# Kernel tuning notes

Hardware: AMD Instinct MI355X
Metric: run time of the kernel (lower is better)

## Reference

```python
import jax, jax.numpy as jnp
import numpy as np

N = 500_000          # total nodes (25000 graphs x 20 joints)
E = 800_000          # total edges (25000 graphs x 32 edges)
NUM_EDGES = 32       # edges per graph (module init arg)
IN_C = 128
OUT_C = 256
LN_EPS = 1e-5


def setup_inputs() -> dict:
    key = jax.random.key(0)
    ks = jax.random.split(key, 8)
    x = jax.random.normal(ks[0], (N, IN_C), dtype=jnp.float32)
    edge_index = jax.random.randint(ks[1], (2, E), 0, N, dtype=jnp.int64)
    # learned per-graph edge weights (init ones in torch; randomized positive here)
    edge_weights = jax.random.uniform(ks[2], (NUM_EDGES,), jnp.float32, 0.5, 1.5)
    W_gcn = jax.random.normal(ks[3], (IN_C, OUT_C), jnp.float32) / np.float32(np.sqrt(IN_C))
    b_gcn = jnp.zeros((OUT_C,), jnp.float32)
    W_res = jax.random.normal(ks[4], (IN_C, OUT_C), jnp.float32) / np.float32(np.sqrt(IN_C))
    b_res = jnp.zeros((OUT_C,), jnp.float32)
    gamma = jnp.ones((OUT_C,), jnp.float32)
    beta = jnp.zeros((OUT_C,), jnp.float32)
    return dict(x=x, edge_weights=edge_weights, W_gcn=W_gcn, b_gcn=b_gcn,
                W_res=W_res, b_res=b_res, gamma=gamma, beta=beta,
                edge_index=edge_index)


def reference(x, edge_weights, W_gcn, b_gcn, W_res, b_res, gamma, beta, edge_index):
    n = x.shape[0]
    e_tot = edge_index.shape[1]
    batch_size = e_tot // NUM_EDGES
    ew = jnp.tile(edge_weights, batch_size)            # repeated per-batch weights [E]
    row, col = edge_index[0], edge_index[1]            # source -> target

    # GCN symmetric normalization with implicit self loops (weight 1)
    deg = jax.ops.segment_sum(ew, col, num_segments=n) + 1.0   # [N]
    dinv = jax.lax.rsqrt(deg)                                   # [N]
    norm = dinv[row] * ew * dinv[col]                           # [E]

    xw = x @ W_gcn                                              # [N, OUT_C]
    agg = jax.ops.segment_sum(norm[:, None] * xw[row], col, num_segments=n)
    # self-loop contribution: norm_ii = dinv_i * 1 * dinv_i = 1/deg_i
    gcn_out = agg + xw * (dinv * dinv)[:, None] + b_gcn         # [N, OUT_C]

    res = x @ W_res + b_res                                     # residual Linear
    h = gcn_out + res

    mu = jnp.mean(h, axis=-1, keepdims=True)
    var = jnp.mean((h - mu) ** 2, axis=-1, keepdims=True)
    hn = (h - mu) * jax.lax.rsqrt(var + LN_EPS)
    return jax.nn.relu(hn * gamma + beta)
```

## Files before the change

kernel.cpp:

```cpp
#include <hip/hip_runtime.h>
#include <hip/hip_bf16.h>

typedef __attribute__((ext_vector_type(8))) short short8;
typedef __attribute__((ext_vector_type(8))) unsigned short ushort8;
typedef __attribute__((ext_vector_type(4))) float f32x4;
typedef unsigned short u16;
typedef unsigned long long u64;

#define IN_C 128
#define OUT_C 256
#define LN_EPS 1e-5f
#define CHUNK 512
#define WSCALE 1048576.0f

__device__ __forceinline__ u16 f2bf(float f) {
    __hip_bfloat16 h = __float2bfloat16(f);
    return __builtin_bit_cast(u16, h);
}

__global__ void k_zero(float4* __restrict__ p, int n4) {
    int i = blockIdx.x * 256 + threadIdx.x;
    if (i < n4) p[i] = make_float4(0.f, 0.f, 0.f, 0.f);
}

__global__ void k_count(const int* __restrict__ ei, const float* __restrict__ ew,
                        u64* __restrict__ pk, int E, int nbc,
                        const float* __restrict__ Wg, const float* __restrict__ Wr,
                        const float* __restrict__ bg, const float* __restrict__ br,
                        u16* __restrict__ wfrag, float* __restrict__ bc) {
    int b = blockIdx.x;
    if (b < nbc) {
        int e = b * 256 + threadIdx.x;
        if (e < E) {
            int c = ei[E + e];
            unsigned w = (unsigned)(ew[e & 31] * WSCALE + 0.5f);
            atomicAdd(&pk[c], (1ULL << 32) | (u64)w);
        }
        return;
    }
    int tid = (b - nbc) * 256 + threadIdx.x;
    if (tid < OUT_C) bc[tid] = bg[tid] + br[tid];
    if (tid >= 8192) return;
    int l = tid & 63;
    int t = (tid >> 6) & 15;
    int s = tid >> 10;
    int n = t * 16 + (l & 15);
    int k0 = s * 32 + (l >> 4) * 8;
    short8 pkk;
#pragma unroll
    for (int j = 0; j < 8; ++j) {
        int k = k0 + j;
        float w = (k < IN_C) ? Wg[k * OUT_C + n] : Wr[(k - IN_C) * OUT_C + n];
        pkk[j] = (short)f2bf(w);
    }
    reinterpret_cast<short8*>(wfrag)[tid] = pkk;
}

__global__ void k_scan1(const u64* __restrict__ pk, int* __restrict__ partial,
                        float* __restrict__ dinv, int n) {
    __shared__ int sm[256];
    int b = blockIdx.x, t = threadIdx.x;
    int base = b * 1024 + t * 4;
    int s = 0;
#pragma unroll
    for (int k = 0; k < 4; ++k) {
        int i = base + k;
        if (i < n) {
            u64 v = pk[i];
            s += (int)(v >> 32);
            dinv[i] = rsqrtf(1.0f + (float)(unsigned)(v & 0xffffffffULL) * (1.0f / WSCALE));
        }
    }
    sm[t] = s; __syncthreads();
    for (int m = 128; m > 0; m >>= 1) { if (t < m) sm[t] += sm[t + m]; __syncthreads(); }
    if (t == 0) partial[b] = sm[0];
}

__global__ void k_scan2(int* __restrict__ partial, int nb) {
    __shared__ int sm[512];
    int t = threadIdx.x;
    sm[t] = (t < nb) ? partial[t] : 0;
    __syncthreads();
    for (int d = 1; d < 512; d <<= 1) {
        int v = (t >= d) ? sm[t - d] : 0;
        __syncthreads();
        sm[t] += v;
        __syncthreads();
    }
    if (t < nb) partial[t] = (t == 0) ? 0 : sm[t - 1];
}

__global__ void k_scan3(const u64* __restrict__ pk, const int* __restrict__ partial,
                        int* __restrict__ off, int* __restrict__ cur, int n, int E) {
    __shared__ int sm[256];
    int b = blockIdx.x, t = threadIdx.x;
    int base = b * 1024 + t * 4;
    int c[4]; int s = 0;
#pragma unroll
    for (int k = 0; k < 4; ++k) {
        int i = base + k;
        c[k] = (i < n) ? (int)(pk[i] >> 32) : 0;
        s += c[k];
    }
    sm[t] = s; __syncthreads();
    for (int d = 1; d < 256; d <<= 1) {
        int v = (t >= d) ? sm[t - d] : 0;
        __syncthreads();
        sm[t] += v;
        __syncthreads();
    }
    int run = partial[b] + (sm[t] - s);
#pragma unroll
    for (int k = 0; k < 4; ++k) {
        int i = base + k;
        if (i < n) { off[i] = run; cur[i] = run; }
        run += c[k];
    }
    if (b == 0 && t == 0) off[n] = E;
}

__global__ void k_place(const int* __restrict__ ei, const float* __restrict__ ew,
                        const float* __restrict__ dinv, int* __restrict__ cur,
                        int2* __restrict__ rec2, int E) {
    int e = blockIdx.x * 256 + threadIdx.x;
    if (e >= E) return;
    int r = ei[e], c = ei[E + e];
    float nrm = dinv[r] * ew[e & 31] * dinv[c];
    int p = atomicAdd(&cur[c], 1);
    rec2[p] = make_int2(r, __float_as_int(nrm));
}

__global__ __launch_bounds__(512, 4) void k_gemm(
    const float4* __restrict__ x4, const float* __restrict__ dinv,
    const int* __restrict__ off, const int2* __restrict__ rec2g,
    const u16* __restrict__ wfrag, const float* __restrict__ bc,
    const float* __restrict__ gamma, const float* __restrict__ beta,
    float* __restrict__ out, int N) {

    __shared__ u16 A[32 * 264];
    __shared__ float red[8 * 32 * 2];
    __shared__ float fin[32 * 2];
    __shared__ int2 recs[CHUNK];

    const int tid = threadIdx.x;
    const int lane = tid & 63;
    const int wv = tid >> 6;
    const long r0 = (long)blockIdx.x * 32;

    const int trow = tid >> 4;
    const int tq = tid & 15;
    const long gr = r0 + trow;

    float ua[8];
    int p0 = 0, p1 = 0;
    {
        u16* xp = &A[trow * 264 + 128 + tq * 8];
        if (gr < N) {
            float d = dinv[gr];
            float d2 = d * d;
            const float4* xs = x4 + gr * 32 + tq * 2;
            float4 v0 = xs[0], v1 = xs[1];
            ushort4 x0, x1;
            x0.x = f2bf(v0.x); x0.y = f2bf(v0.y); x0.z = f2bf(v0.z); x0.w = f2bf(v0.w);
            x1.x = f2bf(v1.x); x1.y = f2bf(v1.y); x1.z = f2bf(v1.z); x1.w = f2bf(v1.w);
            *reinterpret_cast<ushort4*>(xp) = x0;
            *reinterpret_cast<ushort4*>(xp + 4) = x1;
            ua[0] = v0.x * d2; ua[1] = v0.y * d2; ua[2] = v0.z * d2; ua[3] = v0.w * d2;
            ua[4] = v1.x * d2; ua[5] = v1.y * d2; ua[6] = v1.z * d2; ua[7] = v1.w * d2;
            p0 = off[gr]; p1 = off[gr + 1];
        } else {
#pragma unroll
            for (int k = 0; k < 8; ++k) ua[k] = 0.f;
            ushort4 zz = {0, 0, 0, 0};
            *reinterpret_cast<ushort4*>(xp) = zz;
            *reinterpret_cast<ushort4*>(xp + 4) = zz;
        }
    }

    const int rend = (int)((r0 + 32 < N) ? (r0 + 32) : N);
    const int e0 = off[r0];
    const int e1 = off[rend];
    for (int cb = e0; cb < e1; cb += CHUNK) {
        const int ce = (cb + CHUNK < e1) ? (cb + CHUNK) : e1;
        __syncthreads();
        for (int i = tid; i < ce - cb; i += 512) recs[i] = rec2g[cb + i];
        __syncthreads();
        const int q0 = (p0 > cb) ? p0 : cb;
        const int q1 = (p1 < ce) ? p1 : ce;
        for (int p = q0; p < q1; p += 4) {
            const int nb = q1 - p;
            int sr[4]; float nr[4];
            float4 ga[4][2];
#pragma unroll
            for (int b = 0; b < 4; ++b) {
                if (b < nb) {
                    int2 rc = recs[p - cb + b];
                    sr[b] = rc.x;
                    nr[b] = __int_as_float(rc.y);
                }
            }
#pragma unroll
            for (int b = 0; b < 4; ++b) {
                if (b < nb) {
                    const float4* xr = x4 + (long)sr[b] * 32 + tq * 2;
                    ga[b][0] = xr[0];
                    ga[b][1] = xr[1];
                }
            }
#pragma unroll
            for (int b = 0; b < 4; ++b) {
                if (b < nb) {
                    ua[0] += nr[b] * ga[b][0].x; ua[1] += nr[b] * ga[b][0].y;
                    ua[2] += nr[b] * ga[b][0].z; ua[3] += nr[b] * ga[b][0].w;
                    ua[4] += nr[b] * ga[b][1].x; ua[5] += nr[b] * ga[b][1].y;
                    ua[6] += nr[b] * ga[b][1].z; ua[7] += nr[b] * ga[b][1].w;
                }
            }
        }
    }

    {
        ushort4 u0, u1;
        u0.x = f2bf(ua[0]); u0.y = f2bf(ua[1]); u0.z = f2bf(ua[2]); u0.w = f2bf(ua[3]);
        u1.x = f2bf(ua[4]); u1.y = f2bf(ua[5]); u1.z = f2bf(ua[6]); u1.w = f2bf(ua[7]);
        u16* up = &A[trow * 264 + tq * 8];
        *reinterpret_cast<ushort4*>(up) = u0;
        *reinterpret_cast<ushort4*>(up + 4) = u1;
    }
    __syncthreads();

    const short8* wf = reinterpret_cast<const short8*>(wfrag);
    short8 bfr[8][2];
#pragma unroll
    for (int s = 0; s < 8; ++s) {
#pragma unroll
        for (int t = 0; t < 2; ++t)
            bfr[s][t] = wf[(s * 16 + (wv * 2 + t)) * 64 + lane];
    }

    f32x4 acc[2][2];
#pragma unroll
    for (int m = 0; m < 2; ++m)
#pragma unroll
        for (int t = 0; t < 2; ++t) acc[m][t] = (f32x4){0.f, 0.f, 0.f, 0.f};

    const int arowb = lane & 15;
    const int koff = (lane >> 4) * 8;
#pragma unroll
    for (int s = 0; s < 8; ++s) {
#pragma unroll
        for (int m = 0; m < 2; ++m) {
            short8 af = *reinterpret_cast<const short8*>(
                &A[(m * 16 + arowb) * 264 + s * 32 + koff]);
#pragma unroll
            for (int t = 0; t < 2; ++t)
                acc[m][t] = __builtin_amdgcn_mfma_f32_16x16x32_bf16(af, bfr[s][t], acc[m][t], 0, 0, 0);
        }
    }

    const int ncol = lane & 15;
    const int g = lane >> 4;
    const float bc0 = bc[wv * 32 + ncol];
    const float bc1 = bc[wv * 32 + 16 + ncol];
#pragma unroll
    for (int m = 0; m < 2; ++m) {
#pragma unroll
        for (int j = 0; j < 4; ++j) {
            float v0 = acc[m][0][j] + bc0;
            float v1 = acc[m][1][j] + bc1;
            acc[m][0][j] = v0;
            acc[m][1][j] = v1;
            float s = v0 + v1;
            float q = v0 * v0 + v1 * v1;
#pragma unroll
            for (int msk = 1; msk < 16; msk <<= 1) {
                s += __shfl_xor(s, msk);
                q += __shfl_xor(q, msk);
            }
            if (ncol == 0) {
                int row = m * 16 + g * 4 + j;
                red[(wv * 32 + row) * 2 + 0] = s;
                red[(wv * 32 + row) * 2 + 1] = q;
            }
        }
    }
    __syncthreads();
    if (tid < 64) {
        int row = tid >> 1, q = tid & 1;
        float t = 0.f;
#pragma unroll
        for (int w = 0; w < 8; ++w) t += red[(w * 32 + row) * 2 + q];
        fin[row * 2 + q] = t;
    }
    __syncthreads();

    const float gv0 = gamma[wv * 32 + ncol], bv0 = beta[wv * 32 + ncol];
    const float gv1 = gamma[wv * 32 + 16 + ncol], bv1 = beta[wv * 32 + 16 + ncol];
#pragma unroll
    for (int m = 0; m < 2; ++m) {
#pragma unroll
        for (int j = 0; j < 4; ++j) {
            int row = m * 16 + g * 4 + j;
            long rr = r0 + row;
            if (rr < N) {
                float mean = fin[row * 2] * (1.f / 256.f);
                float var = fin[row * 2 + 1] * (1.f / 256.f) - mean * mean;
                float rstd = rsqrtf(var + LN_EPS);
                float o0 = (acc[m][0][j] - mean) * rstd * gv0 + bv0;
                float o1 = (acc[m][1][j] - mean) * rstd * gv1 + bv1;
                float* op = out + rr * (long)OUT_C + wv * 32 + ncol;
                op[0]  = fmaxf(o0, 0.f);
                op[16] = fmaxf(o1, 0.f);
            }
        }
    }
}

extern "C" void kernel_launch(void* const* d_in, const int* in_sizes, int n_in,
                              void* d_out, int out_size, void* d_ws, size_t ws_size,
                              hipStream_t stream) {
    const float* x    = (const float*)d_in[0];
    const float* ew   = (const float*)d_in[1];
    const float* Wg   = (const float*)d_in[2];
    const float* bg   = (const float*)d_in[3];
    const float* Wr   = (const float*)d_in[4];
    const float* br   = (const float*)d_in[5];
    const float* gm   = (const float*)d_in[6];
    const float* bt   = (const float*)d_in[7];
    const int*   ei   = (const int*)d_in[8];

    const int N = in_sizes[0] / IN_C;
    const int E = in_sizes[8] / 2;
    const int NB1 = (N + 1023) / 1024;
    const int NBC = (E + 255) / 256;

    int2*  rec2 = (int2*)d_ws;
    u64*   pk   = (u64*)(rec2 + E);
    float* dinv = (float*)(pk + N);
    int*   off  = (int*)(dinv + N);
    int*   cur  = off + N + 1;
    int*   part = cur + N;
    u16*   wfrag = (u16*)(part + 512);
    float* bc   = (float*)(wfrag + 65536);

    const int n4 = (2 * N + 3) / 4;
    k_zero<<<(n4 + 255) / 256, 256, 0, stream>>>((float4*)pk, n4);
    k_count<<<NBC + 32, 256, 0, stream>>>(ei, ew, pk, E, NBC,
                                          Wg, Wr, bg, br, wfrag, bc);
    k_scan1<<<NB1, 256, 0, stream>>>(pk, part, dinv, N);
    k_scan2<<<1, 512, 0, stream>>>(part, NB1);
    k_scan3<<<NB1, 256, 0, stream>>>(pk, part, off, cur, N, E);
    k_place<<<(E + 255) / 256, 256, 0, stream>>>(ei, ew, dinv, cur, rec2, E);
    k_gemm<<<(N + 31) / 32, 512, 0, stream>>>((const float4*)x, dinv, off, rec2,
                                              wfrag, bc, gm, bt, (float*)d_out, N);
}
```

Before: 410.6 us.

## Halve k_gemm block to 256 threads, each thread gathering two rows

Reduces the fused gather+GEMM+LayerNorm block from 512 to 256 threads, so each thread aggregates neighbours for two node rows and each wave computes 64 output columns instead of 32. Weight fragments are now loaded from global memory inside the MFMA loop rather than preloaded into registers. The goal is higher occupancy, fewer block-level reductions and more memory-level parallelism per thread. The cost is that the two rows' gathers run serially within a thread, and the weight loads in the inner loop may add latency.

```diff
diff --git a/kernel.cpp b/kernel.cpp
--- a/kernel.cpp
+++ b/kernel.cpp
@@ -130,7 +130,7 @@
     rec2[p] = make_int2(r, __float_as_int(nrm));
 }
 
-__global__ __launch_bounds__(512, 4) void k_gemm(
+__global__ __launch_bounds__(256, 8) void k_gemm(
     const float4* __restrict__ x4, const float* __restrict__ dinv,
     const int* __restrict__ off, const int2* __restrict__ rec2g,
     const u16* __restrict__ wfrag, const float* __restrict__ bc,
@@ -138,7 +138,7 @@
     float* __restrict__ out, int N) {
 
     __shared__ u16 A[32 * 264];
-    __shared__ float red[8 * 32 * 2];
+    __shared__ float red[4 * 32 * 2];
     __shared__ float fin[32 * 2];
     __shared__ int2 recs[CHUNK];
 
@@ -149,11 +149,11 @@
 
     const int trow = tid >> 4;
     const int tq = tid & 15;
-    const long gr = r0 + trow;
-
-    float ua[8];
-    int p0 = 0, p1 = 0;
+
+    float uaA[8], uaB[8];
+    int pA0 = 0, pA1 = 0, pB0 = 0, pB1 = 0;
     {
+        const long gr = r0 + trow;
         u16* xp = &A[trow * 264 + 128 + tq * 8];
         if (gr < N) {
             float d = dinv[gr];
@@ -165,12 +165,36 @@
             x1.x = f2bf(v1.x); x1.y = f2bf(v1.y); x1.z = f2bf(v1.z); x1.w = f2bf(v1.w);
             *reinterpret_cast<ushort4*>(xp) = x0;
             *reinterpret_cast<ushort4*>(xp + 4) = x1;
-            ua[0] = v0.x * d2; ua[1] = v0.y * d2; ua[2] = v0.z * d2; ua[3] = v0.w * d2;
-            ua[4] = v1.x * d2; ua[5] = v1.y * d2; ua[6] = v1.z * d2; ua[7] = v1.w * d2;
-            p0 = off[gr]; p1 = off[gr + 1];
+            uaA[0] = v0.x * d2; uaA[1] = v0.y * d2; uaA[2] = v0.z * d2; uaA[3] = v0.w * d2;
+            uaA[4] = v1.x * d2; uaA[5] = v1.y * d2; uaA[6] = v1.z * d2; uaA[7] = v1.w * d2;
+            pA0 = off[gr]; pA1 = off[gr + 1];
         } else {
 #pragma unroll
-            for (int k = 0; k < 8; ++k) ua[k] = 0.f;
+            for (int k = 0; k < 8; ++k) uaA[k] = 0.f;
+            ushort4 zz = {0, 0, 0, 0};
+            *reinterpret_cast<ushort4*>(xp) = zz;
+            *reinterpret_cast<ushort4*>(xp + 4) = zz;
+        }
+    }
+    {
+        const long gr = r0 + trow + 16;
+        u16* xp = &A[(trow + 16) * 264 + 128 + tq * 8];
+        if (gr < N) {
+            float d = dinv[gr];
+            float d2 = d * d;
+            const float4* xs = x4 + gr * 32 + tq * 2;
+            float4 v0 = xs[0], v1 = xs[1];
+            ushort4 x0, x1;
+            x0.x = f2bf(v0.x); x0.y = f2bf(v0.y); x0.z = f2bf(v0.z); x0.w = f2bf(v0.w);
+            x1.x = f2bf(v1.x); x1.y = f2bf(v1.y); x1.z = f2bf(v1.z); x1.w = f2bf(v1.w);
+            *reinterpret_cast<ushort4*>(xp) = x0;
+            *reinterpret_cast<ushort4*>(xp + 4) = x1;
+            uaB[0] = v0.x * d2; uaB[1] = v0.y * d2; uaB[2] = v0.z * d2; uaB[3] = v0.w * d2;
+            uaB[4] = v1.x * d2; uaB[5] = v1.y * d2; uaB[6] = v1.z * d2; uaB[7] = v1.w * d2;
+            pB0 = off[gr]; pB1 = off[gr + 1];
+        } else {
+#pragma unroll
+            for (int k = 0; k < 8; ++k) uaB[k] = 0.f;
             ushort4 zz = {0, 0, 0, 0};
             *reinterpret_cast<ushort4*>(xp) = zz;
             *reinterpret_cast<ushort4*>(xp + 4) = zz;
@@ -183,37 +207,73 @@
     for (int cb = e0; cb < e1; cb += CHUNK) {
         const int ce = (cb + CHUNK < e1) ? (cb + CHUNK) : e1;
         __syncthreads();
-        for (int i = tid; i < ce - cb; i += 512) recs[i] = rec2g[cb + i];
-        __syncthreads();
-        const int q0 = (p0 > cb) ? p0 : cb;
-        const int q1 = (p1 < ce) ? p1 : ce;
-        for (int p = q0; p < q1; p += 4) {
-            const int nb = q1 - p;
-            int sr[4]; float nr[4];
-            float4 ga[4][2];
-#pragma unroll
-            for (int b = 0; b < 4; ++b) {
-                if (b < nb) {
-                    int2 rc = recs[p - cb + b];
-                    sr[b] = rc.x;
-                    nr[b] = __int_as_float(rc.y);
-                }
-            }
-#pragma unroll
-            for (int b = 0; b < 4; ++b) {
-                if (b < nb) {
-                    const float4* xr = x4 + (long)sr[b] * 32 + tq * 2;
-                    ga[b][0] = xr[0];
-                    ga[b][1] = xr[1];
-                }
-            }
-#pragma unroll
-            for (int b = 0; b < 4; ++b) {
-                if (b < nb) {
-                    ua[0] += nr[b] * ga[b][0].x; ua[1] += nr[b] * ga[b][0].y;
-                    ua[2] += nr[b] * ga[b][0].z; ua[3] += nr[b] * ga[b][0].w;
-                    ua[4] += nr[b] * ga[b][1].x; ua[5] += nr[b] * ga[b][1].y;
-                    ua[6] += nr[b] * ga[b][1].z; ua[7] += nr[b] * ga[b][1].w;
+        for (int i = tid; i < ce - cb; i += 256) recs[i] = rec2g[cb + i];
+        __syncthreads();
+        {
+            const int q0 = (pA0 > cb) ? pA0 : cb;
+            const int q1 = (pA1 < ce) ? pA1 : ce;
+            for (int p = q0; p < q1; p += 4) {
+                const int nb = q1 - p;
+                int sr[4]; float nr[4];
+                float4 ga[4][2];
+#pragma unroll
+                for (int b = 0; b < 4; ++b) {
+                    if (b < nb) {
+                        int2 rc = recs[p - cb + b];
+                        sr[b] = rc.x;
+                        nr[b] = __int_as_float(rc.y);
+                    }
+                }
+#pragma unroll
+                for (int b = 0; b < 4; ++b) {
+                    if (b < nb) {
+                        const float4* xr = x4 + (long)sr[b] * 32 + tq * 2;
+                        ga[b][0] = xr[0];
+                        ga[b][1] = xr[1];
+                    }
+                }
+#pragma unroll
+                for (int b = 0; b < 4; ++b) {
+                    if (b < nb) {
+                        uaA[0] += nr[b] * ga[b][0].x; uaA[1] += nr[b] * ga[b][0].y;
+                        uaA[2] += nr[b] * ga[b][0].z; uaA[3] += nr[b] * ga[b][0].w;
+                        uaA[4] += nr[b] * ga[b][1].x; uaA[5] += nr[b] * ga[b][1].y;
+                        uaA[6] += nr[b] * ga[b][1].z; uaA[7] += nr[b] * ga[b][1].w;
+                    }
+                }
+            }
+        }
+        {
+            const int q0 = (pB0 > cb) ? pB0 : cb;
+            const int q1 = (pB1 < ce) ? pB1 : ce;
+            for (int p = q0; p < q1; p += 4) {
+                const int nb = q1 - p;
+                int sr[4]; float nr[4];
+                float4 ga[4][2];
+#pragma unroll
+                for (int b = 0; b < 4; ++b) {
+                    if (b < nb) {
+                        int2 rc = recs[p - cb + b];
+                        sr[b] = rc.x;
+                        nr[b] = __int_as_float(rc.y);
+                    }
+                }
+#pragma unroll
+                for (int b = 0; b < 4; ++b) {
+                    if (b < nb) {
+                        const float4* xr = x4 + (long)sr[b] * 32 + tq * 2;
+                        ga[b][0] = xr[0];
+                        ga[b][1] = xr[1];
+                    }
+                }
+#pragma unroll
+                for (int b = 0; b < 4; ++b) {
+                    if (b < nb) {
+                        uaB[0] += nr[b] * ga[b][0].x; uaB[1] += nr[b] * ga[b][0].y;
+                        uaB[2] += nr[b] * ga[b][0].z; uaB[3] += nr[b] * ga[b][0].w;
+                        uaB[4] += nr[b] * ga[b][1].x; uaB[5] += nr[b] * ga[b][1].y;
+                        uaB[6] += nr[b] * ga[b][1].z; uaB[7] += nr[b] * ga[b][1].w;
+                    }
                 }
             }
         }
@@ -221,31 +281,28 @@
 
     {
         ushort4 u0, u1;
-        u0.x = f2bf(ua[0]); u0.y = f2bf(ua[1]); u0.z = f2bf(ua[2]); u0.w = f2bf(ua[3]);
-        u1.x = f2bf(ua[4]); u1.y = f2bf(ua[5]); u1.z = f2bf(ua[6]); u1.w = f2bf(ua[7]);
+        u0.x = f2bf(uaA[0]); u0.y = f2bf(uaA[1]); u0.z = f2bf(uaA[2]); u0.w = f2bf(uaA[3]);
+        u1.x = f2bf(uaA[4]); u1.y = f2bf(uaA[5]); u1.z = f2bf(uaA[6]); u1.w = f2bf(uaA[7]);
         u16* up = &A[trow * 264 + tq * 8];
         *reinterpret_cast<ushort4*>(up) = u0;
         *reinterpret_cast<ushort4*>(up + 4) = u1;
+        u0.x = f2bf(uaB[0]); u0.y = f2bf(uaB[1]); u0.z = f2bf(uaB[2]); u0.w = f2bf(uaB[3]);
+        u1.x = f2bf(uaB[4]); u1.y = f2bf(uaB[5]); u1.z = f2bf(uaB[6]); u1.w = f2bf(uaB[7]);
+        up = &A[(trow + 16) * 264 + tq * 8];
+        *reinterpret_cast<ushort4*>(up) = u0;
+        *reinterpret_cast<ushort4*>(up + 4) = u1;
     }
     __syncthreads();
 
-    const short8* wf = reinterpret_cast<const short8*>(wfrag);
-    short8 bfr[8][2];
-#pragma unroll
-    for (int s = 0; s < 8; ++s) {
-#pragma unroll
-        for (int t = 0; t < 2; ++t)
-            bfr[s][t] = wf[(s * 16 + (wv * 2 + t)) * 64 + lane];
-    }
-
-    f32x4 acc[2][2];
+    f32x4 acc[2][4];
 #pragma unroll
     for (int m = 0; m < 2; ++m)
 #pragma unroll
-        for (int t = 0; t < 2; ++t) acc[m][t] = (f32x4){0.f, 0.f, 0.f, 0.f};
+        for (int t = 0; t < 4; ++t) acc[m][t] = (f32x4){0.f, 0.f, 0.f, 0.f};
 
     const int arowb = lane & 15;
     const int koff = (lane >> 4) * 8;
+    const short8* wf = reinterpret_cast<const short8*>(wfrag);
 #pragma unroll
     for (int s = 0; s < 8; ++s) {
 #pragma unroll
@@ -253,25 +310,30 @@
             short8 af = *reinterpret_cast<const short8*>(
                 &A[(m * 16 + arowb) * 264 + s * 32 + koff]);
 #pragma unroll
-            for (int t = 0; t < 2; ++t)
-                acc[m][t] = __builtin_amdgcn_mfma_f32_16x16x32_bf16(af, bfr[s][t], acc[m][t], 0, 0, 0);
+            for (int t = 0; t < 4; ++t) {
+                short8 bfr = wf[(s * 16 + (wv * 4 + t)) * 64 + lane];
+                acc[m][t] = __builtin_amdgcn_mfma_f32_16x16x32_bf16(af, bfr, acc[m][t], 0, 0, 0);
+            }
         }
     }
 
     const int ncol = lane & 15;
     const int g = lane >> 4;
-    const float bc0 = bc[wv * 32 + ncol];
-    const float bc1 = bc[wv * 32 + 16 + ncol];
+    float bcv[4];
+#pragma unroll
+    for (int t = 0; t < 4; ++t) bcv[t] = bc[wv * 64 + t * 16 + ncol];
 #pragma unroll
     for (int m = 0; m < 2; ++m) {
 #pragma unroll
         for (int j = 0; j < 4; ++j) {
-            float v0 = acc[m][0][j] + bc0;
-            float v1 = acc[m][1][j] + bc1;
-            acc[m][0][j] = v0;
-            acc[m][1][j] = v1;
-            float s = v0 + v1;
-            float q = v0 * v0 + v1 * v1;
+            float s = 0.f, q = 0.f;
+#pragma unroll
+            for (int t = 0; t < 4; ++t) {
+                float v = acc[m][t][j] + bcv[t];
+                acc[m][t][j] = v;
+                s += v;
+                q += v * v;
+            }
 #pragma unroll
             for (int msk = 1; msk < 16; msk <<= 1) {
                 s += __shfl_xor(s, msk);
@@ -289,13 +351,17 @@
         int row = tid >> 1, q = tid & 1;
         float t = 0.f;
 #pragma unroll
-        for (int w = 0; w < 8; ++w) t += red[(w * 32 + row) * 2 + q];
+        for (int w = 0; w < 4; ++w) t += red[(w * 32 + row) * 2 + q];
         fin[row * 2 + q] = t;
     }
     __syncthreads();
 
-    const float gv0 = gamma[wv * 32 + ncol], bv0 = beta[wv * 32 + ncol];
-    const float gv1 = gamma[wv * 32 + 16 + ncol], bv1 = beta[wv * 32 + 16 + ncol];
+    float gv[4], bv[4];
+#pragma unroll
+    for (int t = 0; t < 4; ++t) {
+        gv[t] = gamma[wv * 64 + t * 16 + ncol];
+        bv[t] = beta[wv * 64 + t * 16 + ncol];
+    }
 #pragma unroll
     for (int m = 0; m < 2; ++m) {
 #pragma unroll
@@ -306,11 +372,12 @@
                 float mean = fin[row * 2] * (1.f / 256.f);
                 float var = fin[row * 2 + 1] * (1.f / 256.f) - mean * mean;
                 float rstd = rsqrtf(var + LN_EPS);
-                float o0 = (acc[m][0][j] - mean) * rstd * gv0 + bv0;
-                float o1 = (acc[m][1][j] - mean) * rstd * gv1 + bv1;
-                float* op = out + rr * (long)OUT_C + wv * 32 + ncol;
-                op[0]  = fmaxf(o0, 0.f);
-                op[16] = fmaxf(o1, 0.f);
+                float* op = out + rr * (long)OUT_C + wv * 64 + ncol;
+#pragma unroll
+                for (int t = 0; t < 4; ++t) {
+                    float o = (acc[m][t][j] - mean) * rstd * gv[t] + bv[t];
+                    op[t * 16] = fmaxf(o, 0.f);
+                }
             }
         }
     }
@@ -351,6 +418,6 @@
     k_scan2<<<1, 512, 0, stream>>>(part, NB1);
     k_scan3<<<NB1, 256, 0, stream>>>(pk, part, off, cur, N, E);
     k_place<<<(E + 255) / 256, 256, 0, stream>>>(ei, ew, dinv, cur, rec2, E);
-    k_gemm<<<(N + 31) / 32, 512, 0, stream>>>((const float4*)x, dinv, off, rec2,
+    k_gemm<<<(N + 31) / 32, 256, 0, stream>>>((const float4*)x, dinv, off, rec2,
                                               wfrag, bc, gm, bt, (float*)d_out, N);
 }
```

After: 424.6 us. +3.4%, slower.
